# Performance work log

Measured on AMD Instinct MI355X. Metric: run time of the kernel, lower is better.

## Reference

```python
import jax, jax.numpy as jnp
import numpy as np

N, E, IN, H, C, ED = 50000, 800000, 128, 4, 64, 4
NEG_SLOPE = 0.2


def setup_inputs() -> dict:
    key = jax.random.key(0)
    ks = iter(jax.random.split(key, 40))
    def p(shape, s=0.05):
        return jax.random.normal(next(ks), shape, jnp.float32) * s
    inp = dict(
        x=jax.random.normal(next(ks), (N, IN), jnp.float32),
        edge_index=jax.random.randint(next(ks), (2, E), 0, N),
        edge_attr=jax.random.normal(next(ks), (E, ED), jnp.float32),
        # GATConv layer 1 (concat=True)
        W1=p((IN, H * C)), att_src1=p((H, C)), att_dst1=p((H, C)),
        We1=p((ED, H * C)), att_e1=p((H, C)), b1=p((H * C,)),
        g1=jnp.ones((H * C,), jnp.float32), be1=jnp.zeros((H * C,), jnp.float32),
        # GATConv layer 2 (concat=False -> mean over heads)
        W2=p((H * C, H * C)), att_src2=p((H, C)), att_dst2=p((H, C)),
        We2=p((ED, H * C)), att_e2=p((H, C)), b2=p((C,)),
        g2=jnp.ones((C,), jnp.float32), be2=jnp.zeros((C,), jnp.float32),
        # skip / MLP head
        skip_W=p((IN, C)), skip_b=p((C,)),
        fc1_W=p((C, C // 2)), fc1_b=p((C // 2,)),
        fc2_W=p((C // 2, 1)), fc2_b=p((1,)),
    )
    return inp


def _add_self_loops(edge_index, edge_attr, n):
    # PyG GATConv default: add_self_loops=True, fill_value='mean'
    src, dst = edge_index[0], edge_index[1]
    sums = jax.ops.segment_sum(edge_attr, dst, num_segments=n)
    cnt = jax.ops.segment_sum(jnp.ones((edge_attr.shape[0], 1), edge_attr.dtype), dst, num_segments=n)
    mean_attr = sums / jnp.maximum(cnt, 1.0)
    loop = jnp.arange(n)
    src = jnp.concatenate([src, loop])
    dst = jnp.concatenate([dst, loop])
    ea = jnp.concatenate([edge_attr, mean_attr], axis=0)
    return src, dst, ea


def _gat_layer(x, src, dst, ea, W, a_src, a_dst, We, a_e, bias, n, concat):
    xs = (x @ W).reshape(n, H, C)                     # [N,H,C]
    alpha_src = (xs * a_src).sum(-1)                  # [N,H]
    alpha_dst = (xs * a_dst).sum(-1)                  # [N,H]
    ep = (ea @ We).reshape(-1, H, C)                  # [Et,H,C]
    alpha_e = (ep * a_e).sum(-1)                      # [Et,H]
    alpha = jax.nn.leaky_relu(alpha_src[src] + alpha_dst[dst] + alpha_e, NEG_SLOPE)
    # segment softmax over destination nodes
    m = jax.ops.segment_max(alpha, dst, num_segments=n)
    alpha = jnp.exp(alpha - m[dst])
    denom = jax.ops.segment_sum(alpha, dst, num_segments=n)
    alpha = alpha / (denom[dst] + 1e-16)
    out = jax.ops.segment_sum(xs[src] * alpha[:, :, None], dst, num_segments=n)  # [N,H,C]
    out = out.reshape(n, H * C) if concat else out.mean(axis=1)
    return out + bias


def _bn(x, g, b):
    mu = x.mean(0)
    var = x.var(0)
    return (x - mu) * jax.lax.rsqrt(var + 1e-5) * g + b


def reference(x, edge_index, edge_attr, W1, att_src1, att_dst1, We1, att_e1, b1, g1, be1,
              W2, att_src2, att_dst2, We2, att_e2, b2, g2, be2,
              skip_W, skip_b, fc1_W, fc1_b, fc2_W, fc2_b):
    n = x.shape[0]
    src, dst, ea = _add_self_loops(edge_index, edge_attr, n)
    residual = x @ skip_W + skip_b
    h = _gat_layer(x, src, dst, ea, W1, att_src1, att_dst1, We1, att_e1, b1, n, True)
    h = jax.nn.elu(_bn(h, g1, be1))
    h = _gat_layer(h, src, dst, ea, W2, att_src2, att_dst2, We2, att_e2, b2, n, False)
    h = jax.nn.elu(_bn(h, g2, be2))
    h = h + residual
    h = jax.nn.relu(h @ fc1_W + fc1_b)
    h = jax.nn.softplus(h @ fc2_W + fc2_b)
    return h.squeeze(-1)
```

## Files before the change

kernel.cpp:

```cpp
#include <hip/hip_runtime.h>
#include <math.h>

static constexpr int N_NODES = 50000;
static constexpr int N_EDGES = 800000;
static constexpr int IN_F = 128;
static constexpr int CH = 64;
static constexpr int HC = 256;
static constexpr float NEG_SLOPE = 0.2f;

typedef __attribute__((ext_vector_type(8))) short bf16x8;
typedef __attribute__((ext_vector_type(4))) float f32x4;

__device__ __forceinline__ unsigned pack_bf(float a, float b) {
    unsigned ua = __float_as_uint(a) + 0x8000u;
    unsigned ub = __float_as_uint(b) + 0x8000u;
    return __builtin_amdgcn_perm(ub, ua, 0x07060302u);
}
__device__ __forceinline__ float bflo(unsigned u) { return __uint_as_float(u << 16); }
__device__ __forceinline__ float bfhi(unsigned u) { return __uint_as_float(u & 0xffff0000u); }
__device__ __forceinline__ float bfs(unsigned short u) {
    return __uint_as_float((unsigned)u << 16);
}
__device__ __forceinline__ float elu(float v) { return v > 0.f ? v : expm1f(v); }

__device__ __forceinline__ int sigma(int p) { return ((p & 15) << 4) | (p >> 4); }

__global__ void csr_hist(const int* __restrict__ ei, int* __restrict__ deg) {
    int e = blockIdx.x * blockDim.x + threadIdx.x;
    if (e >= N_EDGES) return;
    atomicAdd(&deg[ei[N_EDGES + e]], 1);
}

__global__ void scan_block(const int* __restrict__ deg, int* __restrict__ rowptr,
                           int* __restrict__ bsum) {
    __shared__ int s[256];
    int tid = threadIdx.x;
    int i = blockIdx.x * 256 + tid;
    int v = (i < N_NODES) ? deg[i] : 0;
    s[tid] = v;
    __syncthreads();
    for (int off = 1; off < 256; off <<= 1) {
        int t = (tid >= off) ? s[tid - off] : 0;
        __syncthreads();
        s[tid] += t;
        __syncthreads();
    }
    if (i < N_NODES) rowptr[i] = s[tid] - v;
    if (tid == 255) bsum[blockIdx.x] = s[255];
}

__global__ void scan_bsum(int* __restrict__ bsum, int nb) {
    __shared__ int s[256];
    int tid = threadIdx.x;
    int v = (tid < nb) ? bsum[tid] : 0;
    s[tid] = v;
    __syncthreads();
    for (int off = 1; off < 256; off <<= 1) {
        int t = (tid >= off) ? s[tid - off] : 0;
        __syncthreads();
        s[tid] += t;
        __syncthreads();
    }
    if (tid < nb) bsum[tid] = s[tid] - v;
}

__global__ void scan_add(int* __restrict__ rowptr, const int* __restrict__ bsum,
                         int* __restrict__ fillc) {
    int i = blockIdx.x * blockDim.x + threadIdx.x;
    if (i < N_NODES) {
        rowptr[i] += bsum[i >> 8];
        fillc[i] = 0;
    }
    if (i == N_NODES) rowptr[N_NODES] = N_EDGES;
}

__global__ void csr_fill(const int* __restrict__ ei, const int* __restrict__ rowptr,
                         int* __restrict__ fillc, int* __restrict__ csr_src,
                         int* __restrict__ pos) {
    int e = blockIdx.x * blockDim.x + threadIdx.x;
    if (e >= N_EDGES) return;
    int s = ei[e];
    int t = ei[N_EDGES + e];
    int p = atomicAdd(&fillc[t], 1);
    int i = rowptr[t] + p;
    csr_src[i] = s;
    pos[e] = i;
}

__global__ void conv_all(const float* __restrict__ W1, const float* __restrict__ W2,
                         const float* __restrict__ Ws, const float* __restrict__ We1,
                         const float* __restrict__ atte1, const float* __restrict__ We2,
                         const float* __restrict__ atte2, unsigned short* __restrict__ WT1,
                         unsigned short* __restrict__ WT2, unsigned short* __restrict__ WTs,
                         float* __restrict__ weff) {
    int t = blockIdx.x * blockDim.x + threadIdx.x;
    if (t < 32768) {
        int k = t >> 8, n = t & 255;
        unsigned u = __float_as_uint(W1[t]) + 0x8000u;
        WT1[n * 128 + k] = (unsigned short)(u >> 16);
    } else if (t < 98304) {
        int u2 = t - 32768;
        int k = u2 >> 8, n = u2 & 255;
        unsigned u = __float_as_uint(W2[u2]) + 0x8000u;
        WT2[n * 256 + sigma(k)] = (unsigned short)(u >> 16);
    } else if (t < 106496) {
        int u2 = t - 98304;
        int k = u2 >> 6, n = u2 & 63;
        unsigned u = __float_as_uint(Ws[u2]) + 0x8000u;
        WTs[n * 128 + k] = (unsigned short)(u >> 16);
    } else if (t < 106496 + 32) {
        int idx = t - 106496;
        const float* We = idx < 16 ? We1 : We2;
        const float* ae = idx < 16 ? atte1 : atte2;
        int j = idx & 15;
        int d = j >> 2, h = j & 3;
        float s = 0.f;
        for (int c = 0; c < CH; ++c) s += We[d * HC + h * CH + c] * ae[h * CH + c];
        weff[idx] = s;
    }
}

template <int K, bool ABF, bool BN>
__global__ __launch_bounds__(256) void gemm_mfma_att(
    const void* __restrict__ Av, const unsigned short* __restrict__ BT,
    const float* __restrict__ scale, const float* __restrict__ shift,
    const float* __restrict__ att_src, const float* __restrict__ att_dst,
    unsigned short* __restrict__ xsb, float* __restrict__ asrc, float* __restrict__ adst,
    int M) {
    constexpr int RT = 2, NT = 16;
    const int lane = threadIdx.x & 63;
    const int wid = threadIdx.x >> 6;
    const int r0 = blockIdx.x * (4 * RT * 16) + wid * RT * 16;
    const int lr = lane & 15;
    const int kg = lane >> 4;
    f32x4 acc[RT][NT] = {};
    const float* af = (const float*)Av;
    const unsigned short* ab = (const unsigned short*)Av;
    size_t rowoff[RT];
#pragma unroll
    for (int m = 0; m < RT; ++m) {
        int r = r0 + m * 16 + lr;
        if (r >= M) r = M - 1;
        rowoff[m] = (size_t)r * K + kg * 8;
    }
    const unsigned short* brow = BT + (size_t)lr * K + kg * 8;
    for (int k0 = 0; k0 < K; k0 += 32) {
        float4 sc0, sc1, sh0, sh1;
        if constexpr (BN) {
            sc0 = *reinterpret_cast<const float4*>(scale + k0 + kg * 8);
            sc1 = *reinterpret_cast<const float4*>(scale + k0 + kg * 8 + 4);
            sh0 = *reinterpret_cast<const float4*>(shift + k0 + kg * 8);
            sh1 = *reinterpret_cast<const float4*>(shift + k0 + kg * 8 + 4);
        }
        bf16x8 a[RT];
#pragma unroll
        for (int m = 0; m < RT; ++m) {
            if constexpr (!ABF) {
                const float4 lo = *reinterpret_cast<const float4*>(af + rowoff[m] + k0);
                const float4 hi = *reinterpret_cast<const float4*>(af + rowoff[m] + k0 + 4);
                union { bf16x8 v; unsigned u[4]; } fa;
                fa.u[0] = pack_bf(lo.x, lo.y);
                fa.u[1] = pack_bf(lo.z, lo.w);
                fa.u[2] = pack_bf(hi.x, hi.y);
                fa.u[3] = pack_bf(hi.z, hi.w);
                a[m] = fa.v;
            } else {
                union { bf16x8 v; unsigned short us[8]; unsigned u[4]; } fa;
                fa.v = *reinterpret_cast<const bf16x8*>(ab + rowoff[m] + k0);
                if constexpr (BN) {
                    float f0 = elu(fmaf(bfs(fa.us[0]), sc0.x, sh0.x));
                    float f1 = elu(fmaf(bfs(fa.us[1]), sc0.y, sh0.y));
                    float f2 = elu(fmaf(bfs(fa.us[2]), sc0.z, sh0.z));
                    float f3 = elu(fmaf(bfs(fa.us[3]), sc0.w, sh0.w));
                    float f4 = elu(fmaf(bfs(fa.us[4]), sc1.x, sh1.x));
                    float f5 = elu(fmaf(bfs(fa.us[5]), sc1.y, sh1.y));
                    float f6 = elu(fmaf(bfs(fa.us[6]), sc1.z, sh1.z));
                    float f7 = elu(fmaf(bfs(fa.us[7]), sc1.w, sh1.w));
                    fa.u[0] = pack_bf(f0, f1);
                    fa.u[1] = pack_bf(f2, f3);
                    fa.u[2] = pack_bf(f4, f5);
                    fa.u[3] = pack_bf(f6, f7);
                }
                a[m] = fa.v;
            }
        }
#pragma unroll
        for (int c = 0; c < NT; ++c) {
            bf16x8 b = *reinterpret_cast<const bf16x8*>(brow + (size_t)c * 16 * K + k0);
#pragma unroll
            for (int m = 0; m < RT; ++m)
                acc[m][c] = __builtin_amdgcn_mfma_f32_16x16x32_bf16(a[m], b, acc[m][c], 0, 0, 0);
        }
    }
    float attS[NT], attD[NT];
#pragma unroll
    for (int c = 0; c < NT; ++c) {
        attS[c] = att_src[c * 16 + lr];
        attD[c] = att_dst[c * 16 + lr];
    }
#pragma unroll
    for (int m = 0; m < RT; ++m) {
#pragma unroll
        for (int j = 0; j < 4; ++j) {
            int row = r0 + m * 16 + kg * 4 + j;
            bool valid = row < M;
            uint4 ua, ub;
            ua.x = pack_bf(acc[m][0][j], acc[m][1][j]);
            ua.y = pack_bf(acc[m][2][j], acc[m][3][j]);
            ua.z = pack_bf(acc[m][4][j], acc[m][5][j]);
            ua.w = pack_bf(acc[m][6][j], acc[m][7][j]);
            ub.x = pack_bf(acc[m][8][j], acc[m][9][j]);
            ub.y = pack_bf(acc[m][10][j], acc[m][11][j]);
            ub.z = pack_bf(acc[m][12][j], acc[m][13][j]);
            ub.w = pack_bf(acc[m][14][j], acc[m][15][j]);
            if (valid) {
                uint4* dst = reinterpret_cast<uint4*>(xsb + (size_t)row * HC) + lr * 2;
                dst[0] = ua;
                dst[1] = ub;
            }
#pragma unroll
            for (int h = 0; h < 4; ++h) {
                float ps = acc[m][4 * h + 0][j] * attS[4 * h + 0] +
                           acc[m][4 * h + 1][j] * attS[4 * h + 1] +
                           acc[m][4 * h + 2][j] * attS[4 * h + 2] +
                           acc[m][4 * h + 3][j] * attS[4 * h + 3];
                float pd = acc[m][4 * h + 0][j] * attD[4 * h + 0] +
                           acc[m][4 * h + 1][j] * attD[4 * h + 1] +
                           acc[m][4 * h + 2][j] * attD[4 * h + 2] +
                           acc[m][4 * h + 3][j] * attD[4 * h + 3];
#pragma unroll
                for (int mk = 1; mk < 16; mk <<= 1) {
                    ps += __shfl_xor(ps, mk);
                    pd += __shfl_xor(pd, mk);
                }
                if (valid && lr == 0) {
                    asrc[row * 4 + h] = ps;
                    adst[row * 4 + h] = pd;
                }
            }
        }
    }
}

template <int K, int NT, int RT>
__global__ __launch_bounds__(256) void gemm_mfma_bias(const float* __restrict__ A,
                                                      const unsigned short* __restrict__ BT,
                                                      const float* __restrict__ bias,
                                                      float* __restrict__ C, int M) {
    const int lane = threadIdx.x & 63;
    const int wid = threadIdx.x >> 6;
    const int r0 = blockIdx.x * (4 * RT * 16) + wid * RT * 16;
    const int lr = lane & 15;
    const int kg = lane >> 4;
    f32x4 acc[RT][NT] = {};
    const float* arow[RT];
#pragma unroll
    for (int m = 0; m < RT; ++m) {
        int r = r0 + m * 16 + lr;
        if (r >= M) r = M - 1;
        arow[m] = A + (size_t)r * K + kg * 8;
    }
    const unsigned short* brow = BT + (size_t)lr * K + kg * 8;
    for (int k0 = 0; k0 < K; k0 += 32) {
        bf16x8 a[RT];
#pragma unroll
        for (int m = 0; m < RT; ++m) {
            const float4 lo = *reinterpret_cast<const float4*>(arow[m] + k0);
            const float4 hi = *reinterpret_cast<const float4*>(arow[m] + k0 + 4);
            union { bf16x8 v; unsigned u[4]; } fa;
            fa.u[0] = pack_bf(lo.x, lo.y);
            fa.u[1] = pack_bf(lo.z, lo.w);
            fa.u[2] = pack_bf(hi.x, hi.y);
            fa.u[3] = pack_bf(hi.z, hi.w);
            a[m] = fa.v;
        }
#pragma unroll
        for (int c = 0; c < NT; ++c) {
            bf16x8 b = *reinterpret_cast<const bf16x8*>(brow + (size_t)c * 16 * K + k0);
#pragma unroll
            for (int m = 0; m < RT; ++m)
                acc[m][c] = __builtin_amdgcn_mfma_f32_16x16x32_bf16(a[m], b, acc[m][c], 0, 0, 0);
        }
    }
#pragma unroll
    for (int m = 0; m < RT; ++m) {
        int rbase = r0 + m * 16 + kg * 4;
#pragma unroll
        for (int c = 0; c < NT; ++c) {
            int col = c * 16 + lr;
            float bv = bias[col];
#pragma unroll
            for (int j = 0; j < 4; ++j) {
                int r = rbase + j;
                if (r < M) C[(size_t)r * (NT * 16) + col] = acc[m][c][j] + bv;
            }
        }
    }
}

__global__ __launch_bounds__(256) void edge_w(
    const int* __restrict__ ei, const float4* __restrict__ ea, const int* __restrict__ pos,
    const float* __restrict__ weff, const float4* __restrict__ asrcv,
    const float4* __restrict__ adstv, uint4* __restrict__ pw) {
    int e = blockIdx.x * blockDim.x + threadIdx.x;
    if (e >= N_EDGES) return;
    int s = ei[e];
    int t = ei[N_EDGES + e];
    const float4 v = ea[e];
    const float4 as4 = asrcv[s];
    const float4 ad4 = adstv[t];
    const float asl[4] = {as4.x, as4.y, as4.z, as4.w};
    const float adl[4] = {ad4.x, ad4.y, ad4.z, ad4.w};
    float p[4], aev[4];
#pragma unroll
    for (int h = 0; h < 4; ++h) {
        float ae = v.x * weff[h] + v.y * weff[4 + h] + v.z * weff[8 + h] + v.w * weff[12 + h];
        float l = asl[h] + adl[h] + ae;
        l = fmaxf(l, NEG_SLOPE * l);
        p[h] = __expf(l);
        aev[h] = ae;
    }
    pw[pos[e]] = make_uint4(pack_bf(p[0], p[1]), pack_bf(p[2], p[3]),
                            pack_bf(aev[0], aev[1]), pack_bf(aev[2], aev[3]));
}

template <bool MEAN>
__global__ __launch_bounds__(256) void gat_node(
    const int* __restrict__ rowptr, const int* __restrict__ csr_src,
    const uint4* __restrict__ pw, const float4* __restrict__ asrcv,
    const float4* __restrict__ adstv, const uint2* __restrict__ xsb,
    void* __restrict__ outp) {
    int t = blockIdx.x * 4 + (threadIdx.x >> 6);
    if (t >= N_NODES) return;
    const int lane = threadIdx.x & 63;
    const int h = lane & 3;
    const unsigned sh = (h & 1) ? 0u : 16u;
    const bool hiW = (h & 2) != 0;
    const int start = rowptr[t], end = rowptr[t + 1];
    const int deg = end - start;
    const uint2* xl = xsb + lane;
    float acc0 = 0.f, acc1 = 0.f, acc2 = 0.f, acc3 = 0.f;
    float psum = 0.f, aesum = 0.f;
    int i = start;
    for (; i + 8 <= end; i += 8) {
        uint2 f[8];
        float p[8], ae[8];
#pragma unroll
        for (int j = 0; j < 8; ++j) {
            int s = csr_src[i + j];
            f[j] = xl[(size_t)s * 64];
            const uint4 w = pw[i + j];
            unsigned pword = hiW ? w.y : w.x;
            unsigned aeword = hiW ? w.w : w.z;
            p[j] = __uint_as_float((pword << sh) & 0xffff0000u);
            ae[j] = __uint_as_float((aeword << sh) & 0xffff0000u);
        }
#pragma unroll
        for (int j = 0; j < 8; ++j) {
            psum += p[j];
            aesum += ae[j];
            acc0 += bflo(f[j].x) * p[j];
            acc1 += bfhi(f[j].x) * p[j];
            acc2 += bflo(f[j].y) * p[j];
            acc3 += bfhi(f[j].y) * p[j];
        }
    }
    for (; i < end; ++i) {
        int s = csr_src[i];
        uint2 f = xl[(size_t)s * 64];
        const uint4 w = pw[i];
        unsigned pword = hiW ? w.y : w.x;
        unsigned aeword = hiW ? w.w : w.z;
        float p = __uint_as_float((pword << sh) & 0xffff0000u);
        float ae = __uint_as_float((aeword << sh) & 0xffff0000u);
        psum += p;
        aesum += ae;
        acc0 += bflo(f.x) * p;
        acc1 += bfhi(f.x) * p;
        acc2 += bflo(f.y) * p;
        acc3 += bfhi(f.y) * p;
    }
    const float inv_deg = deg > 0 ? 1.0f / (float)deg : 1.0f;
    const float4 as4 = asrcv[t];
    const float4 ad4 = adstv[t];
    float asl = h == 0 ? as4.x : h == 1 ? as4.y : h == 2 ? as4.z : as4.w;
    float adl = h == 0 ? ad4.x : h == 1 ? ad4.y : h == 2 ? ad4.z : ad4.w;
    float l = asl + adl + aesum * inv_deg;
    l = fmaxf(l, NEG_SLOPE * l);
    const float pself = __expf(l);
    uint2 sf = xl[(size_t)t * 64];
    acc0 += bflo(sf.x) * pself;
    acc1 += bfhi(sf.x) * pself;
    acc2 += bflo(sf.y) * pself;
    acc3 += bfhi(sf.y) * pself;
    const float inv = 1.0f / (psum + pself + 1e-16f);
    acc0 *= inv; acc1 *= inv; acc2 *= inv; acc3 *= inv;
    if constexpr (MEAN) {
        acc0 += __shfl_xor(acc0, 1); acc0 += __shfl_xor(acc0, 2);
        acc1 += __shfl_xor(acc1, 1); acc1 += __shfl_xor(acc1, 2);
        acc2 += __shfl_xor(acc2, 1); acc2 += __shfl_xor(acc2, 2);
        acc3 += __shfl_xor(acc3, 1); acc3 += __shfl_xor(acc3, 2);
        if (h == 0) {
            int q = lane >> 2;
            float* o = reinterpret_cast<float*>(outp) + (size_t)t * CH + q;
            o[0] = 0.25f * acc0;
            o[16] = 0.25f * acc1;
            o[32] = 0.25f * acc2;
            o[48] = 0.25f * acc3;
        }
    } else {
        reinterpret_cast<uint2*>(outp)[(size_t)t * 64 + lane] =
            make_uint2(pack_bf(acc0, acc1), pack_bf(acc2, acc3));
    }
}

__global__ void colstats_bf(const unsigned short* __restrict__ X, float* __restrict__ sum,
                            float* __restrict__ sumsq, int M) {
    int c = threadIdx.x;
    int r0 = blockIdx.x * 256;
    int r1 = min(M, r0 + 256);
    float s = 0.f, q = 0.f;
    for (int r = r0; r < r1; ++r) {
        float v = bfs(X[(size_t)r * HC + c]);
        s += v;
        q += v * v;
    }
    atomicAdd(&sum[c], s);
    atomicAdd(&sumsq[c], q);
}

template <int F>
__global__ void colstats(const float* __restrict__ X, float* __restrict__ sum,
                         float* __restrict__ sumsq, int M) {
    const int NG = 256 / F;
    int c = threadIdx.x % F;
    int g = threadIdx.x / F;
    int r0 = blockIdx.x * 256;
    int r1 = min(M, r0 + 256);
    float s = 0.f, q = 0.f;
    for (int r = r0 + g; r < r1; r += NG) {
        float v = X[(size_t)r * F + c];
        s += v;
        q += v * v;
    }
    atomicAdd(&sum[c], s);
    atomicAdd(&sumsq[c], q);
}

template <bool PERM>
__global__ void bn_finalize(const float* __restrict__ sum, const float* __restrict__ sumsq,
                            const float* __restrict__ g, const float* __restrict__ be,
                            float* __restrict__ scale, float* __restrict__ shift, int F,
                            float invM) {
    int c = blockIdx.x * blockDim.x + threadIdx.x;
    if (c >= F) return;
    int tc = PERM ? sigma(c) : c;
    float mean = sum[c] * invM;
    float var = sumsq[c] * invM - mean * mean;
    float sc = g[tc] * rsqrtf(var + 1e-5f);
    scale[c] = sc;
    shift[c] = be[tc] - mean * sc;
}

__global__ __launch_bounds__(256) void head_mlp(
    const float* __restrict__ h2, const float* __restrict__ scale,
    const float* __restrict__ shift, const float* __restrict__ residual,
    const float* __restrict__ fc1W, const float* __restrict__ fc1b,
    const float* __restrict__ fc2W, const float* __restrict__ fc2b,
    float* __restrict__ out) {
    int n = blockIdx.x * 4 + (threadIdx.x >> 6);
    if (n >= N_NODES) return;
    int w = threadIdx.x >> 6;
    int lane = threadIdx.x & 63;
    __shared__ float hrow[4][64];
    float v = fmaf(h2[(size_t)n * CH + lane], scale[lane], shift[lane]);
    v = elu(v) + residual[(size_t)n * CH + lane];
    hrow[w][lane] = v;
    float p = 0.f;
    if (lane < 32) {
        float acc = fc1b[lane];
#pragma unroll
        for (int k = 0; k < CH; ++k) acc = fmaf(hrow[w][k], fc1W[k * 32 + lane], acc);
        acc = fmaxf(acc, 0.f);
        p = acc * fc2W[lane];
    }
    for (int off = 16; off > 0; off >>= 1) p += __shfl_down(p, off);
    if (lane == 0) {
        float z = p + fc2b[0];
        out[n] = z > 20.f ? z : log1pf(expf(z));
    }
}

extern "C" void kernel_launch(void* const* d_in, const int* in_sizes, int n_in, void* d_out,
                              int out_size, void* d_ws, size_t ws_size, hipStream_t stream) {
    const float* x        = (const float*)d_in[0];
    const int*   ei       = (const int*)d_in[1];
    const float* ea       = (const float*)d_in[2];
    const float* W1       = (const float*)d_in[3];
    const float* att_src1 = (const float*)d_in[4];
    const float* att_dst1 = (const float*)d_in[5];
    const float* We1      = (const float*)d_in[6];
    const float* att_e1   = (const float*)d_in[7];
    const float* g1       = (const float*)d_in[9];
    const float* be1      = (const float*)d_in[10];
    const float* W2       = (const float*)d_in[11];
    const float* att_src2 = (const float*)d_in[12];
    const float* att_dst2 = (const float*)d_in[13];
    const float* We2      = (const float*)d_in[14];
    const float* att_e2   = (const float*)d_in[15];
    const float* g2       = (const float*)d_in[17];
    const float* be2      = (const float*)d_in[18];
    const float* skip_W   = (const float*)d_in[19];
    const float* skip_b   = (const float*)d_in[20];
    const float* fc1_W    = (const float*)d_in[21];
    const float* fc1_b    = (const float*)d_in[22];
    const float* fc2_W    = (const float*)d_in[23];
    const float* fc2_b    = (const float*)d_in[24];
    float* out = (float*)d_out;

    float* wsf = (float*)d_ws;
    size_t off = 0;
    auto take = [&](size_t n) {
        float* p = wsf + off;
        off += n;
        return p;
    };
    unsigned short* xsb  = (unsigned short*)take((size_t)N_NODES * HC / 2);
    unsigned short* aggb = (unsigned short*)take((size_t)N_NODES * HC / 2);
    uint4* pw       = (uint4*)take((size_t)N_EDGES * 4);
    int* csr_src    = (int*)take(N_EDGES);
    int* pos        = (int*)take(N_EDGES);
    int* rowptr     = (int*)take(N_NODES + 1);
    int* degfill    = (int*)take(N_NODES);
    int* bsum       = (int*)take(256);
    float* asrc     = take(N_NODES * 4);
    float* adst     = take(N_NODES * 4);
    float* residual = take((size_t)N_NODES * CH);
    float* h2       = take((size_t)N_NODES * CH);
    float* weff     = take(32);
    float* colsum   = take(HC);
    float* colsq    = take(HC);
    float* scaleb   = take(HC);
    float* shiftb   = take(HC);
    unsigned short* WT1 = (unsigned short*)take(IN_F * HC / 2);
    unsigned short* WT2 = (unsigned short*)take(HC * HC / 2);
    unsigned short* WTs = (unsigned short*)take(IN_F * CH / 2);

    const int EB = (N_EDGES + 255) / 256;
    const int NBLK = (N_NODES + 255) / 256;
    const int NODE4 = (N_NODES + 3) / 4;

    hipMemsetAsync(degfill, 0, N_NODES * sizeof(int), stream);
    csr_hist<<<EB, 256, 0, stream>>>(ei, degfill);
    scan_block<<<NBLK, 256, 0, stream>>>(degfill, rowptr, bsum);
    scan_bsum<<<1, 256, 0, stream>>>(bsum, NBLK);
    scan_add<<<(N_NODES + 256) / 256, 256, 0, stream>>>(rowptr, bsum, degfill);
    csr_fill<<<EB, 256, 0, stream>>>(ei, rowptr, degfill, csr_src, pos);

    conv_all<<<(106528 + 255) / 256, 256, 0, stream>>>(W1, W2, skip_W, We1, att_e1, We2,
                                                       att_e2, WT1, WT2, WTs, weff);

    gemm_mfma_bias<IN_F, 4, 4><<<(N_NODES + 255) / 256, 256, 0, stream>>>(
        x, WTs, skip_b, residual, N_NODES);

    gemm_mfma_att<IN_F, false, false><<<(N_NODES + 127) / 128, 256, 0, stream>>>(
        x, WT1, nullptr, nullptr, att_src1, att_dst1, xsb, asrc, adst, N_NODES);
    edge_w<<<EB, 256, 0, stream>>>(ei, (const float4*)ea, pos, weff, (const float4*)asrc,
                                   (const float4*)adst, pw);
    gat_node<false><<<NODE4, 256, 0, stream>>>(rowptr, csr_src, pw, (const float4*)asrc,
                                               (const float4*)adst, (const uint2*)xsb, aggb);
    hipMemsetAsync(colsum, 0, 2 * HC * sizeof(float), stream);
    colstats_bf<<<NBLK, 256, 0, stream>>>(aggb, colsum, colsq, N_NODES);
    bn_finalize<true><<<1, HC, 0, stream>>>(colsum, colsq, g1, be1, scaleb, shiftb, HC,
                                            1.0f / N_NODES);

    gemm_mfma_att<HC, true, true><<<(N_NODES + 127) / 128, 256, 0, stream>>>(
        aggb, WT2, scaleb, shiftb, att_src2, att_dst2, xsb, asrc, adst, N_NODES);
    edge_w<<<EB, 256, 0, stream>>>(ei, (const float4*)ea, pos, weff + 16, (const float4*)asrc,
                                   (const float4*)adst, pw);
    gat_node<true><<<NODE4, 256, 0, stream>>>(rowptr, csr_src, pw, (const float4*)asrc,
                                              (const float4*)adst, (const uint2*)xsb, h2);
    hipMemsetAsync(colsum, 0, 2 * HC * sizeof(float), stream);
    colstats<CH><<<NBLK, 256, 0, stream>>>(h2, colsum, colsq, N_NODES);
    bn_finalize<false><<<1, CH, 0, stream>>>(colsum, colsq, g2, be2, scaleb, shiftb, CH,
                                             1.0f / N_NODES);

    head_mlp<<<NODE4, 256, 0, stream>>>(h2, scaleb, shiftb, residual, fc1_W, fc1_b,
                                        fc2_W, fc2_b, out);
}
```

Baseline: 547.0 us.

## Fuse small setup kernels and skip GEMM into neighbouring kernels to cut launches

Merges the degree histogram with weight conversion, merges the two scan-fix kernels, folds the skip-connection GEMM into the layer-1 attention GEMM so x is read once, and computes BN scale/shift inside the consumer kernels instead of separate finalize launches. Colsum zeroing moves from memset into gat_node block 0. ELU switches from expm1f to __expf-1, which loses some accuracy near zero. The larger accumulator set in the fused GEMM raises register pressure.

Measured after the change: 508.1 us. 7.1% less time.

```diff
diff --git a/kernel.cpp b/kernel.cpp
--- a/kernel.cpp
+++ b/kernel.cpp
@@ -21,79 +21,27 @@
 __device__ __forceinline__ float bfs(unsigned short u) {
     return __uint_as_float((unsigned)u << 16);
 }
-__device__ __forceinline__ float elu(float v) { return v > 0.f ? v : expm1f(v); }
+__device__ __forceinline__ float elu(float v) { return v > 0.f ? v : __expf(v) - 1.0f; }
 
 __device__ __forceinline__ int sigma(int p) { return ((p & 15) << 4) | (p >> 4); }
 
-__global__ void csr_hist(const int* __restrict__ ei, int* __restrict__ deg) {
-    int e = blockIdx.x * blockDim.x + threadIdx.x;
-    if (e >= N_EDGES) return;
-    atomicAdd(&deg[ei[N_EDGES + e]], 1);
-}
-
-__global__ void scan_block(const int* __restrict__ deg, int* __restrict__ rowptr,
-                           int* __restrict__ bsum) {
-    __shared__ int s[256];
-    int tid = threadIdx.x;
-    int i = blockIdx.x * 256 + tid;
-    int v = (i < N_NODES) ? deg[i] : 0;
-    s[tid] = v;
-    __syncthreads();
-    for (int off = 1; off < 256; off <<= 1) {
-        int t = (tid >= off) ? s[tid - off] : 0;
-        __syncthreads();
-        s[tid] += t;
-        __syncthreads();
-    }
-    if (i < N_NODES) rowptr[i] = s[tid] - v;
-    if (tid == 255) bsum[blockIdx.x] = s[255];
-}
-
-__global__ void scan_bsum(int* __restrict__ bsum, int nb) {
-    __shared__ int s[256];
-    int tid = threadIdx.x;
-    int v = (tid < nb) ? bsum[tid] : 0;
-    s[tid] = v;
-    __syncthreads();
-    for (int off = 1; off < 256; off <<= 1) {
-        int t = (tid >= off) ? s[tid - off] : 0;
-        __syncthreads();
-        s[tid] += t;
-        __syncthreads();
-    }
-    if (tid < nb) bsum[tid] = s[tid] - v;
-}
-
-__global__ void scan_add(int* __restrict__ rowptr, const int* __restrict__ bsum,
-                         int* __restrict__ fillc) {
-    int i = blockIdx.x * blockDim.x + threadIdx.x;
-    if (i < N_NODES) {
-        rowptr[i] += bsum[i >> 8];
-        fillc[i] = 0;
-    }
-    if (i == N_NODES) rowptr[N_NODES] = N_EDGES;
-}
-
-__global__ void csr_fill(const int* __restrict__ ei, const int* __restrict__ rowptr,
-                         int* __restrict__ fillc, int* __restrict__ csr_src,
-                         int* __restrict__ pos) {
-    int e = blockIdx.x * blockDim.x + threadIdx.x;
-    if (e >= N_EDGES) return;
-    int s = ei[e];
-    int t = ei[N_EDGES + e];
-    int p = atomicAdd(&fillc[t], 1);
-    int i = rowptr[t] + p;
-    csr_src[i] = s;
-    pos[e] = i;
-}
-
-__global__ void conv_all(const float* __restrict__ W1, const float* __restrict__ W2,
-                         const float* __restrict__ Ws, const float* __restrict__ We1,
-                         const float* __restrict__ atte1, const float* __restrict__ We2,
-                         const float* __restrict__ atte2, unsigned short* __restrict__ WT1,
-                         unsigned short* __restrict__ WT2, unsigned short* __restrict__ WTs,
-                         float* __restrict__ weff) {
-    int t = blockIdx.x * blockDim.x + threadIdx.x;
+static constexpr int EB_BLK = (N_EDGES + 255) / 256;
+static constexpr int CONV_ITEMS = 106496 + 32;
+static constexpr int CONV_BLK = (CONV_ITEMS + 255) / 256;
+
+__global__ void hist_conv(const int* __restrict__ ei, int* __restrict__ deg,
+                          const float* __restrict__ W1, const float* __restrict__ W2,
+                          const float* __restrict__ Ws, const float* __restrict__ We1,
+                          const float* __restrict__ atte1, const float* __restrict__ We2,
+                          const float* __restrict__ atte2, unsigned short* __restrict__ WT1,
+                          unsigned short* __restrict__ WT2, unsigned short* __restrict__ WTs,
+                          float* __restrict__ weff) {
+    if (blockIdx.x < EB_BLK) {
+        int e = blockIdx.x * 256 + threadIdx.x;
+        if (e < N_EDGES) atomicAdd(&deg[ei[N_EDGES + e]], 1);
+        return;
+    }
+    int t = (blockIdx.x - EB_BLK) * 256 + threadIdx.x;
     if (t < 32768) {
         int k = t >> 8, n = t & 255;
         unsigned u = __float_as_uint(W1[t]) + 0x8000u;
@@ -120,20 +68,88 @@
     }
 }
 
-template <int K, bool ABF, bool BN>
+__global__ void scan_block(const int* __restrict__ deg, int* __restrict__ rowptr,
+                           int* __restrict__ bsum) {
+    __shared__ int s[256];
+    int tid = threadIdx.x;
+    int i = blockIdx.x * 256 + tid;
+    int v = (i < N_NODES) ? deg[i] : 0;
+    s[tid] = v;
+    __syncthreads();
+    for (int off = 1; off < 256; off <<= 1) {
+        int t = (tid >= off) ? s[tid - off] : 0;
+        __syncthreads();
+        s[tid] += t;
+        __syncthreads();
+    }
+    if (i < N_NODES) rowptr[i] = s[tid] - v;
+    if (tid == 255) bsum[blockIdx.x] = s[255];
+}
+
+__global__ void scan_add2(int* __restrict__ rowptr, const int* __restrict__ bsum,
+                          int* __restrict__ fillc, int nb) {
+    __shared__ int s[256];
+    int tid = threadIdx.x;
+    int v = (tid < nb) ? bsum[tid] : 0;
+    s[tid] = v;
+    __syncthreads();
+    for (int off = 1; off < 256; off <<= 1) {
+        int t = (tid >= off) ? s[tid - off] : 0;
+        __syncthreads();
+        s[tid] += t;
+        __syncthreads();
+    }
+    int boff = (blockIdx.x == 0) ? 0 : s[blockIdx.x - 1];
+    int i = blockIdx.x * 256 + tid;
+    if (i < N_NODES) {
+        rowptr[i] += boff;
+        fillc[i] = 0;
+    }
+    if (i == N_NODES) rowptr[N_NODES] = N_EDGES;
+}
+
+__global__ void csr_fill(const int* __restrict__ ei, const int* __restrict__ rowptr,
+                         int* __restrict__ fillc, int* __restrict__ csr_src,
+                         int* __restrict__ pos) {
+    int e = blockIdx.x * blockDim.x + threadIdx.x;
+    if (e >= N_EDGES) return;
+    int s = ei[e];
+    int t = ei[N_EDGES + e];
+    int p = atomicAdd(&fillc[t], 1);
+    int i = rowptr[t] + p;
+    csr_src[i] = s;
+    pos[e] = i;
+}
+
+template <int K, bool ABF, bool BN, bool SKIP>
 __global__ __launch_bounds__(256) void gemm_mfma_att(
     const void* __restrict__ Av, const unsigned short* __restrict__ BT,
-    const float* __restrict__ scale, const float* __restrict__ shift,
+    const float* __restrict__ colsum, const float* __restrict__ g,
+    const float* __restrict__ be, float invM,
+    const unsigned short* __restrict__ BTs, const float* __restrict__ skip_b,
+    float* __restrict__ residual,
     const float* __restrict__ att_src, const float* __restrict__ att_dst,
     unsigned short* __restrict__ xsb, float* __restrict__ asrc, float* __restrict__ adst,
     int M) {
     constexpr int RT = 2, NT = 16;
+    __shared__ float s_scale[256], s_shift[256];
+    if constexpr (BN) {
+        int c = threadIdx.x;
+        int tc = sigma(c);
+        float mean = colsum[c] * invM;
+        float var = colsum[256 + c] * invM - mean * mean;
+        float sc = g[tc] * rsqrtf(var + 1e-5f);
+        s_scale[c] = sc;
+        s_shift[c] = be[tc] - mean * sc;
+        __syncthreads();
+    }
     const int lane = threadIdx.x & 63;
     const int wid = threadIdx.x >> 6;
     const int r0 = blockIdx.x * (4 * RT * 16) + wid * RT * 16;
     const int lr = lane & 15;
     const int kg = lane >> 4;
     f32x4 acc[RT][NT] = {};
+    f32x4 accS[RT][4] = {};
     const float* af = (const float*)Av;
     const unsigned short* ab = (const unsigned short*)Av;
     size_t rowoff[RT];
@@ -144,13 +160,14 @@
         rowoff[m] = (size_t)r * K + kg * 8;
     }
     const unsigned short* brow = BT + (size_t)lr * K + kg * 8;
+    const unsigned short* brow_s = SKIP ? BTs + (size_t)lr * K + kg * 8 : nullptr;
     for (int k0 = 0; k0 < K; k0 += 32) {
         float4 sc0, sc1, sh0, sh1;
         if constexpr (BN) {
-            sc0 = *reinterpret_cast<const float4*>(scale + k0 + kg * 8);
-            sc1 = *reinterpret_cast<const float4*>(scale + k0 + kg * 8 + 4);
-            sh0 = *reinterpret_cast<const float4*>(shift + k0 + kg * 8);
-            sh1 = *reinterpret_cast<const float4*>(shift + k0 + kg * 8 + 4);
+            sc0 = *reinterpret_cast<const float4*>(&s_scale[k0 + kg * 8]);
+            sc1 = *reinterpret_cast<const float4*>(&s_scale[k0 + kg * 8 + 4]);
+            sh0 = *reinterpret_cast<const float4*>(&s_shift[k0 + kg * 8]);
+            sh1 = *reinterpret_cast<const float4*>(&s_shift[k0 + kg * 8 + 4]);
         }
         bf16x8 a[RT];
 #pragma unroll
@@ -191,6 +208,16 @@
             for (int m = 0; m < RT; ++m)
                 acc[m][c] = __builtin_amdgcn_mfma_f32_16x16x32_bf16(a[m], b, acc[m][c], 0, 0, 0);
         }
+        if constexpr (SKIP) {
+#pragma unroll
+            for (int c = 0; c < 4; ++c) {
+                bf16x8 b = *reinterpret_cast<const bf16x8*>(brow_s + (size_t)c * 16 * K + k0);
+#pragma unroll
+                for (int m = 0; m < RT; ++m)
+                    accS[m][c] =
+                        __builtin_amdgcn_mfma_f32_16x16x32_bf16(a[m], b, accS[m][c], 0, 0, 0);
+            }
+        }
     }
     float attS[NT], attD[NT];
 #pragma unroll
@@ -218,6 +245,15 @@
                 dst[0] = ua;
                 dst[1] = ub;
             }
+            if constexpr (SKIP) {
+                if (valid) {
+#pragma unroll
+                    for (int c = 0; c < 4; ++c) {
+                        int col = c * 16 + lr;
+                        residual[(size_t)row * CH + col] = accS[m][c][j] + skip_b[col];
+                    }
+                }
+            }
 #pragma unroll
             for (int h = 0; h < 4; ++h) {
                 float ps = acc[m][4 * h + 0][j] * attS[4 * h + 0] +
@@ -237,62 +273,6 @@
                     asrc[row * 4 + h] = ps;
                     adst[row * 4 + h] = pd;
                 }
-            }
-        }
-    }
-}
-
-template <int K, int NT, int RT>
-__global__ __launch_bounds__(256) void gemm_mfma_bias(const float* __restrict__ A,
-                                                      const unsigned short* __restrict__ BT,
-                                                      const float* __restrict__ bias,
-                                                      float* __restrict__ C, int M) {
-    const int lane = threadIdx.x & 63;
-    const int wid = threadIdx.x >> 6;
-    const int r0 = blockIdx.x * (4 * RT * 16) + wid * RT * 16;
-    const int lr = lane & 15;
-    const int kg = lane >> 4;
-    f32x4 acc[RT][NT] = {};
-    const float* arow[RT];
-#pragma unroll
-    for (int m = 0; m < RT; ++m) {
-        int r = r0 + m * 16 + lr;
-        if (r >= M) r = M - 1;
-        arow[m] = A + (size_t)r * K + kg * 8;
-    }
-    const unsigned short* brow = BT + (size_t)lr * K + kg * 8;
-    for (int k0 = 0; k0 < K; k0 += 32) {
-        bf16x8 a[RT];
-#pragma unroll
-        for (int m = 0; m < RT; ++m) {
-            const float4 lo = *reinterpret_cast<const float4*>(arow[m] + k0);
-            const float4 hi = *reinterpret_cast<const float4*>(arow[m] + k0 + 4);
-            union { bf16x8 v; unsigned u[4]; } fa;
-            fa.u[0] = pack_bf(lo.x, lo.y);
-            fa.u[1] = pack_bf(lo.z, lo.w);
-            fa.u[2] = pack_bf(hi.x, hi.y);
-            fa.u[3] = pack_bf(hi.z, hi.w);
-            a[m] = fa.v;
-        }
-#pragma unroll
-        for (int c = 0; c < NT; ++c) {
-            bf16x8 b = *reinterpret_cast<const bf16x8*>(brow + (size_t)c * 16 * K + k0);
-#pragma unroll
-            for (int m = 0; m < RT; ++m)
-                acc[m][c] = __builtin_amdgcn_mfma_f32_16x16x32_bf16(a[m], b, acc[m][c], 0, 0, 0);
-        }
-    }
-#pragma unroll
-    for (int m = 0; m < RT; ++m) {
-        int rbase = r0 + m * 16 + kg * 4;
-#pragma unroll
-        for (int c = 0; c < NT; ++c) {
-            int col = c * 16 + lr;
-            float bv = bias[col];
-#pragma unroll
-            for (int j = 0; j < 4; ++j) {
-                int r = rbase + j;
-                if (r < M) C[(size_t)r * (NT * 16) + col] = acc[m][c][j] + bv;
             }
         }
     }
@@ -329,7 +309,11 @@
     const int* __restrict__ rowptr, const int* __restrict__ csr_src,
     const uint4* __restrict__ pw, const float4* __restrict__ asrcv,
     const float4* __restrict__ adstv, const uint2* __restrict__ xsb,
-    void* __restrict__ outp) {
+    float* __restrict__ zbuf, void* __restrict__ outp) {
+    if (blockIdx.x == 0) {
+        zbuf[threadIdx.x] = 0.f;
+        zbuf[256 + threadIdx.x] = 0.f;
+    }
     int t = blockIdx.x * 4 + (threadIdx.x >> 6);
     if (t >= N_NODES) return;
     const int lane = threadIdx.x & 63;
@@ -447,33 +431,28 @@
     atomicAdd(&sumsq[c], q);
 }
 
-template <bool PERM>
-__global__ void bn_finalize(const float* __restrict__ sum, const float* __restrict__ sumsq,
-                            const float* __restrict__ g, const float* __restrict__ be,
-                            float* __restrict__ scale, float* __restrict__ shift, int F,
-                            float invM) {
-    int c = blockIdx.x * blockDim.x + threadIdx.x;
-    if (c >= F) return;
-    int tc = PERM ? sigma(c) : c;
-    float mean = sum[c] * invM;
-    float var = sumsq[c] * invM - mean * mean;
-    float sc = g[tc] * rsqrtf(var + 1e-5f);
-    scale[c] = sc;
-    shift[c] = be[tc] - mean * sc;
-}
-
 __global__ __launch_bounds__(256) void head_mlp(
-    const float* __restrict__ h2, const float* __restrict__ scale,
-    const float* __restrict__ shift, const float* __restrict__ residual,
-    const float* __restrict__ fc1W, const float* __restrict__ fc1b,
-    const float* __restrict__ fc2W, const float* __restrict__ fc2b,
-    float* __restrict__ out) {
+    const float* __restrict__ h2, const float* __restrict__ colsum,
+    const float* __restrict__ g2, const float* __restrict__ be2, float invM,
+    const float* __restrict__ residual, const float* __restrict__ fc1W,
+    const float* __restrict__ fc1b, const float* __restrict__ fc2W,
+    const float* __restrict__ fc2b, float* __restrict__ out) {
+    __shared__ float s_sc[CH], s_sh[CH];
+    if (threadIdx.x < CH) {
+        int c = threadIdx.x;
+        float mean = colsum[c] * invM;
+        float var = colsum[256 + c] * invM - mean * mean;
+        float sc = g2[c] * rsqrtf(var + 1e-5f);
+        s_sc[c] = sc;
+        s_sh[c] = be2[c] - mean * sc;
+    }
+    __syncthreads();
     int n = blockIdx.x * 4 + (threadIdx.x >> 6);
     if (n >= N_NODES) return;
     int w = threadIdx.x >> 6;
     int lane = threadIdx.x & 63;
     __shared__ float hrow[4][64];
-    float v = fmaf(h2[(size_t)n * CH + lane], scale[lane], shift[lane]);
+    float v = fmaf(h2[(size_t)n * CH + lane], s_sc[lane], s_sh[lane]);
     v = elu(v) + residual[(size_t)n * CH + lane];
     hrow[w][lane] = v;
     float p = 0.f;
@@ -540,51 +519,41 @@
     float* weff     = take(32);
     float* colsum   = take(HC);
     float* colsq    = take(HC);
-    float* scaleb   = take(HC);
-    float* shiftb   = take(HC);
     unsigned short* WT1 = (unsigned short*)take(IN_F * HC / 2);
     unsigned short* WT2 = (unsigned short*)take(HC * HC / 2);
     unsigned short* WTs = (unsigned short*)take(IN_F * CH / 2);
 
-    const int EB = (N_EDGES + 255) / 256;
     const int NBLK = (N_NODES + 255) / 256;
     const int NODE4 = (N_NODES + 3) / 4;
+    const float invM = 1.0f / N_NODES;
 
     hipMemsetAsync(degfill, 0, N_NODES * sizeof(int), stream);
-    csr_hist<<<EB, 256, 0, stream>>>(ei, degfill);
+    hist_conv<<<EB_BLK + CONV_BLK, 256, 0, stream>>>(ei, degfill, W1, W2, skip_W, We1,
+                                                     att_e1, We2, att_e2, WT1, WT2, WTs, weff);
     scan_block<<<NBLK, 256, 0, stream>>>(degfill, rowptr, bsum);
-    scan_bsum<<<1, 256, 0, stream>>>(bsum, NBLK);
-    scan_add<<<(N_NODES + 256) / 256, 256, 0, stream>>>(rowptr, bsum, degfill);
-    csr_fill<<<EB, 256, 0, stream>>>(ei, rowptr, degfill, csr_src, pos);
-
-    conv_all<<<(106528 + 255) / 256, 256, 0, stream>>>(W1, W2, skip_W, We1, att_e1, We2,
-                                                       att_e2, WT1, WT2, WTs, weff);
-
-    gemm_mfma_bias<IN_F, 4, 4><<<(N_NODES + 255) / 256, 256, 0, stream>>>(
-        x, WTs, skip_b, residual, N_NODES);
-
-    gemm_mfma_att<IN_F, false, false><<<(N_NODES + 127) / 128, 256, 0, stream>>>(
-        x, WT1, nullptr, nullptr, att_src1, att_dst1, xsb, asrc, adst, N_NODES);
-    edge_w<<<EB, 256, 0, stream>>>(ei, (const float4*)ea, pos, weff, (const float4*)asrc,
-                                   (const float4*)adst, pw);
+    scan_add2<<<(N_NODES + 256) / 256, 256, 0, stream>>>(rowptr, bsum, degfill, NBLK);
+    csr_fill<<<EB_BLK, 256, 0, stream>>>(ei, rowptr, degfill, csr_src, pos);
+
+    gemm_mfma_att<IN_F, false, false, true><<<(N_NODES + 127) / 128, 256, 0, stream>>>(
+        x, WT1, nullptr, nullptr, nullptr, 0.f, WTs, skip_b, residual, att_src1, att_dst1,
+        xsb, asrc, adst, N_NODES);
+    edge_w<<<EB_BLK, 256, 0, stream>>>(ei, (const float4*)ea, pos, weff, (const float4*)asrc,
+                                       (const float4*)adst, pw);
     gat_node<false><<<NODE4, 256, 0, stream>>>(rowptr, csr_src, pw, (const float4*)asrc,
-                                               (const float4*)adst, (const uint2*)xsb, aggb);
-    hipMemsetAsync(colsum, 0, 2 * HC * sizeof(float), stream);
+                                               (const float4*)adst, (const uint2*)xsb,
+                                               colsum, aggb);
     colstats_bf<<<NBLK, 256, 0, stream>>>(aggb, colsum, colsq, N_NODES);
-    bn_finalize<true><<<1, HC, 0, stream>>>(colsum, colsq, g1, be1, scaleb, shiftb, HC,
-                                            1.0f / N_NODES);
-
-    gemm_mfma_att<HC, true, true><<<(N_NODES + 127) / 128, 256, 0, stream>>>(
-        aggb, WT2, scaleb, shiftb, att_src2, att_dst2, xsb, asrc, adst, N_NODES);
-    edge_w<<<EB, 256, 0, stream>>>(ei, (const float4*)ea, pos, weff + 16, (const float4*)asrc,
-                                   (const float4*)adst, pw);
+
+    gemm_mfma_att<HC, true, true, false><<<(N_NODES + 127) / 128, 256, 0, stream>>>(
+        aggb, WT2, colsum, g1, be1, invM, nullptr, nullptr, nullptr, att_src2, att_dst2,
+        xsb, asrc, adst, N_NODES);
+    edge_w<<<EB_BLK, 256, 0, stream>>>(ei, (const float4*)ea, pos, weff + 16,
+                                       (const float4*)asrc, (const float4*)adst, pw);
     gat_node<true><<<NODE4, 256, 0, stream>>>(rowptr, csr_src, pw, (const float4*)asrc,
-                                              (const float4*)adst, (const uint2*)xsb, h2);
-    hipMemsetAsync(colsum, 0, 2 * HC * sizeof(float), stream);
+                                              (const float4*)adst, (const uint2*)xsb,
+                                              colsum, h2);
     colstats<CH><<<NBLK, 256, 0, stream>>>(h2, colsum, colsq, N_NODES);
-    bn_finalize<false><<<1, CH, 0, stream>>>(colsum, colsq, g2, be2, scaleb, shiftb, CH,
-                                             1.0f / N_NODES);
-
-    head_mlp<<<NODE4, 256, 0, stream>>>(h2, scaleb, shiftb, residual, fc1_W, fc1_b,
+
+    head_mlp<<<NODE4, 256, 0, stream>>>(h2, colsum, g2, be2, invM, residual, fc1_W, fc1_b,
                                         fc2_W, fc2_b, out);
 }
```
